# Performance work log

Measured on AMD Instinct MI355X. Metric: run time of the kernel, lower is better.

Reference implementation:

```python
import jax, jax.numpy as jnp
import numpy as np

N_NODES = 50000
N_EDGES = 600000
D = 128
L = 3


def setup_inputs() -> dict:
    key = jax.random.key(0)
    ks = jax.random.split(key, 6)
    x = jax.random.normal(ks[0], (N_NODES, D), dtype=jnp.float32)
    edge_index = jax.random.randint(ks[1], (2, N_EDGES), 0, N_NODES, dtype=jnp.int64)
    # Glorot-ish scale for 128x128 linears
    s = 1.0 / np.sqrt(D)
    W_l = jax.random.normal(ks[2], (L, D, D), dtype=jnp.float32) * s
    b_l = jnp.zeros((L, D), dtype=jnp.float32)
    W_r = jax.random.normal(ks[3], (L, D, D), dtype=jnp.float32) * s
    W_out = jax.random.normal(ks[4], (D, 1), dtype=jnp.float32) * s
    b_out = jnp.zeros((1,), dtype=jnp.float32)
    return {"x": x, "edge_index": edge_index, "W_l": W_l, "b_l": b_l,
            "W_r": W_r, "W_out": W_out, "b_out": b_out}


def reference(x, edge_index, W_l, b_l, W_r, W_out, b_out):
    # PyG SAGEConv (aggr='mean', root_weight=True):
    #   out_i = lin_l(mean_{j: (j->i)} x_j) + lin_r(x_i)
    src = edge_index[0]
    dst = edge_index[1]
    n = x.shape[0]
    deg = jax.ops.segment_sum(jnp.ones(src.shape, x.dtype), dst, num_segments=n)
    inv_deg = (1.0 / jnp.maximum(deg, 1.0))[:, None]  # [N,1]
    h = x
    for i in range(W_l.shape[0]):  # fixed small layer count
        agg = jax.ops.segment_sum(h[src], dst, num_segments=n) * inv_deg  # [N,D]
        h = agg @ W_l[i] + b_l[i] + h @ W_r[i]
        h = jax.nn.relu(h)  # dropout is identity at eval (p=0.0)
    return (h @ W_out + b_out)[:, 0]  # squeeze(-1) -> [N]
```

## Files before the change

### kernel.cpp

```cpp
#include <hip/hip_runtime.h>

#define N_NODES 50000
#define N_EDGES 600000
#define D 128
#define NLAYERS 3
#define ELL_W 64

typedef __attribute__((ext_vector_type(8))) short short8;
typedef __attribute__((ext_vector_type(4))) float floatx4;

__device__ __forceinline__ float bf_lo(unsigned u) { return __uint_as_float(u << 16); }
__device__ __forceinline__ float bf_hi(unsigned u) { return __uint_as_float(u & 0xffff0000u); }
__device__ __forceinline__ unsigned short f2bf(float f) {
    unsigned u = __float_as_uint(f);
    return (unsigned short)((u + 0x7fffu + ((u >> 16) & 1u)) >> 16);
}


#define CVT_A (N_NODES * D / 4)
#define CVT_B (NLAYERS * D * 256)
#define CVT_D (N_NODES * ELL_W / 4)
#define CVT_TOTAL (CVT_A + CVT_B + N_NODES + CVT_D)

__global__ void cvt_init_kernel(const float* __restrict__ x, const float* __restrict__ Wl,
                                const float* __restrict__ Wr,
                                unsigned short* __restrict__ xb,
                                unsigned short* __restrict__ hb1,
                                unsigned short* __restrict__ hb2,
                                unsigned short* __restrict__ WtF,
                                int* __restrict__ cursor, int* __restrict__ ell) {
    int i = blockIdx.x * blockDim.x + threadIdx.x;
    if (i < CVT_A) {
        float4 v = ((const float4*)x)[i];
        ushort4 o;
        o.x = f2bf(v.x); o.y = f2bf(v.y); o.z = f2bf(v.z); o.w = f2bf(v.w);
        ((ushort4*)xb)[i] = o;
    } else if (i < CVT_A + CVT_B) {
        int t = i - CVT_A;
        int l = t >> 15;
        int r = t & 32767;
        int f = r >> 3;
        int ii = r & 7;
        int jkt = f >> 6;
        int lane = f & 63;
        int j = jkt >> 3;
        int kt = jkt & 7;
        int half = lane & 15;
        int quad = lane >> 4;
        int n = j * 16 + half;
        int k = kt * 32 + quad * 8 + ii;
        float v = (k < D) ? Wl[(size_t)l * D * D + (size_t)k * D + n]
                          : Wr[(size_t)l * D * D + (size_t)(k - D) * D + n];
        WtF[t] = f2bf(v);
    } else if (i < CVT_A + CVT_B + N_NODES) {
        int j = i - (CVT_A + CVT_B);
        cursor[j] = 0;
        if (j < D) {
            xb[(size_t)N_NODES * D + j] = 0;
            hb1[(size_t)N_NODES * D + j] = 0;
            hb2[(size_t)N_NODES * D + j] = 0;
        }
    } else if (i < CVT_TOTAL) {
        int t = i - (CVT_A + CVT_B + N_NODES);
        int4 s = {N_NODES, N_NODES, N_NODES, N_NODES};
        ((int4*)ell)[t] = s;
    }
}


__global__ void fill_kernel(const int* __restrict__ src, const int* __restrict__ dst,
                            int* __restrict__ cursor, int* __restrict__ ell) {
    int e = blockIdx.x * blockDim.x + threadIdx.x;
    if (e < N_EDGES) {
        int d_ = dst[e];
        int pos = atomicAdd(&cursor[d_], 1);
        if (pos < ELL_W) ell[(size_t)d_ * ELL_W + pos] = src[e];
    }
}


template <bool LAST>
__global__ __launch_bounds__(256) void fused_layer_kernel(
    const unsigned short* __restrict__ hin,
    const int* __restrict__ degc, const int* __restrict__ ell,
    const unsigned short* __restrict__ WtF, const float* __restrict__ bias,
    unsigned short* __restrict__ hout,
    const float* __restrict__ Wout, const float* __restrict__ bout,
    float* __restrict__ out) {
    __shared__ union {
        unsigned short a[32 * 256];
        unsigned short c[32][136];
        float red[32][4];
    } sh;

    int m0 = blockIdx.x * 32;
    int tid = threadIdx.x;

    #pragma unroll
    for (int it = 0; it < 2; ++it) {
        int t = it * 256 + tid;
        int rl = t >> 4;
        int c = t & 15;
        int row = min(m0 + rl, N_NODES - 1);
        uint4 v = *((const uint4*)(hin + (size_t)row * D + c * 8));
        int chunk = (16 + c) ^ (rl & 7);
        *((uint4*)&sh.a[rl * 256 + chunk * 8]) = v;
    }

    {
        int grp = tid >> 4;
        int q = tid & 15;
        for (int half_ = 0; half_ < 2; ++half_) {
            int nl = grp + half_ * 16;
            int node = m0 + nl;
            float a[8] = {0.f, 0.f, 0.f, 0.f, 0.f, 0.f, 0.f, 0.f};
            float b[8] = {0.f, 0.f, 0.f, 0.f, 0.f, 0.f, 0.f, 0.f};
            float w = 0.f;
            if (node < N_NODES) {
                int d = min(degc[node], ELL_W);
                int pd = (d + 3) & ~3;
                int beg = node * ELL_W;
                for (int e = beg; e < beg + pd; e += 16) {
                    int cnt = min(beg + pd - e, 16);
                    int idx = ell[e + q];
                    for (int j = 0; j < cnt; j += 4) {
                        int s0 = __shfl(idx, j + 0, 16);
                        int s1 = __shfl(idx, j + 1, 16);
                        int s2 = __shfl(idx, j + 2, 16);
                        int s3 = __shfl(idx, j + 3, 16);
                        uint4 v0 = *((const uint4*)(hin + (size_t)s0 * D + q * 8));
                        uint4 v1 = *((const uint4*)(hin + (size_t)s1 * D + q * 8));
                        uint4 v2 = *((const uint4*)(hin + (size_t)s2 * D + q * 8));
                        uint4 v3 = *((const uint4*)(hin + (size_t)s3 * D + q * 8));
                        a[0] += bf_lo(v0.x); a[1] += bf_hi(v0.x);
                        a[2] += bf_lo(v0.y); a[3] += bf_hi(v0.y);
                        a[4] += bf_lo(v0.z); a[5] += bf_hi(v0.z);
                        a[6] += bf_lo(v0.w); a[7] += bf_hi(v0.w);
                        b[0] += bf_lo(v1.x); b[1] += bf_hi(v1.x);
                        b[2] += bf_lo(v1.y); b[3] += bf_hi(v1.y);
                        b[4] += bf_lo(v1.z); b[5] += bf_hi(v1.z);
                        b[6] += bf_lo(v1.w); b[7] += bf_hi(v1.w);
                        a[0] += bf_lo(v2.x); a[1] += bf_hi(v2.x);
                        a[2] += bf_lo(v2.y); a[3] += bf_hi(v2.y);
                        a[4] += bf_lo(v2.z); a[5] += bf_hi(v2.z);
                        a[6] += bf_lo(v2.w); a[7] += bf_hi(v2.w);
                        b[0] += bf_lo(v3.x); b[1] += bf_hi(v3.x);
                        b[2] += bf_lo(v3.y); b[3] += bf_hi(v3.y);
                        b[4] += bf_lo(v3.z); b[5] += bf_hi(v3.z);
                        b[6] += bf_lo(v3.w); b[7] += bf_hi(v3.w);
                    }
                }
                w = 1.0f / (float)max(d, 1);
            }
            uint4 o;
            o.x = (unsigned)f2bf((a[0] + b[0]) * w) | ((unsigned)f2bf((a[1] + b[1]) * w) << 16);
            o.y = (unsigned)f2bf((a[2] + b[2]) * w) | ((unsigned)f2bf((a[3] + b[3]) * w) << 16);
            o.z = (unsigned)f2bf((a[4] + b[4]) * w) | ((unsigned)f2bf((a[5] + b[5]) * w) << 16);
            o.w = (unsigned)f2bf((a[6] + b[6]) * w) | ((unsigned)f2bf((a[7] + b[7]) * w) << 16);
            int chunk = q ^ (nl & 7);
            *((uint4*)&sh.a[nl * 256 + chunk * 8]) = o;
        }
    }
    __syncthreads();

    int wv = tid >> 6;
    int lane = tid & 63;
    int half = lane & 15;
    int quad = lane >> 4;

    floatx4 acc[2][2];
    #pragma unroll
    for (int mt = 0; mt < 2; mt++)
        #pragma unroll
        for (int jj = 0; jj < 2; jj++)
            acc[mt][jj] = (floatx4){0.f, 0.f, 0.f, 0.f};

    const short8* Bf = (const short8*)WtF;
    #pragma unroll
    for (int kt = 0; kt < 8; kt++) {
        int ch = (kt * 4 + quad) ^ (half & 7);
        short8 a0 = *((const short8*)&sh.a[half * 256 + ch * 8]);
        short8 a1 = *((const short8*)&sh.a[(16 + half) * 256 + ch * 8]);
        #pragma unroll
        for (int jj = 0; jj < 2; jj++) {
            int j = wv * 2 + jj;
            short8 b = Bf[(j * 8 + kt) * 64 + lane];
            acc[0][jj] = __builtin_amdgcn_mfma_f32_16x16x32_bf16(a0, b, acc[0][jj], 0, 0, 0);
            acc[1][jj] = __builtin_amdgcn_mfma_f32_16x16x32_bf16(a1, b, acc[1][jj], 0, 0, 0);
        }
    }
    __syncthreads();

    if (!LAST) {
        #pragma unroll
        for (int jj = 0; jj < 2; jj++) {
            int col = (wv * 2 + jj) * 16 + half;
            float bv = bias[col];
            #pragma unroll
            for (int mt = 0; mt < 2; mt++)
                #pragma unroll
                for (int r = 0; r < 4; r++)
                    sh.c[mt * 16 + quad * 4 + r][col] = f2bf(fmaxf(acc[mt][jj][r] + bv, 0.f));
        }
        __syncthreads();
        #pragma unroll
        for (int it = 0; it < 2; ++it) {
            int t = it * 256 + tid;
            int rl = t >> 4;
            int c = t & 15;
            int row = m0 + rl;
            if (row < N_NODES)
                *((uint4*)(hout + (size_t)row * D + c * 8)) = *((const uint4*)&sh.c[rl][c * 8]);
        }
    } else {
        float vout[2][4] = {{0.f, 0.f, 0.f, 0.f}, {0.f, 0.f, 0.f, 0.f}};
        #pragma unroll
        for (int jj = 0; jj < 2; jj++) {
            int col = (wv * 2 + jj) * 16 + half;
            float bv = bias[col];
            float wo = Wout[col];
            #pragma unroll
            for (int mt = 0; mt < 2; mt++)
                #pragma unroll
                for (int r = 0; r < 4; r++)
                    vout[mt][r] += fmaxf(acc[mt][jj][r] + bv, 0.f) * wo;
        }
        #pragma unroll
        for (int off = 1; off < 16; off <<= 1) {
            #pragma unroll
            for (int mt = 0; mt < 2; mt++)
                #pragma unroll
                for (int r = 0; r < 4; r++)
                    vout[mt][r] += __shfl_xor(vout[mt][r], off, 64);
        }
        if (half == 0) {
            #pragma unroll
            for (int mt = 0; mt < 2; mt++)
                #pragma unroll
                for (int r = 0; r < 4; r++)
                    sh.red[mt * 16 + quad * 4 + r][wv] = vout[mt][r];
        }
        __syncthreads();
        if (tid < 32) {
            int row = m0 + tid;
            if (row < N_NODES)
                out[row] = sh.red[tid][0] + sh.red[tid][1] +
                           sh.red[tid][2] + sh.red[tid][3] + bout[0];
        }
    }
}


extern "C" void kernel_launch(void* const* d_in, const int* in_sizes, int n_in,
                              void* d_out, int out_size, void* d_ws, size_t ws_size,
                              hipStream_t stream) {
    const float* x     = (const float*)d_in[0];
    const int*   edge  = (const int*)d_in[1];
    const float* W_l   = (const float*)d_in[2];
    const float* b_l   = (const float*)d_in[3];
    const float* W_r   = (const float*)d_in[4];
    const float* W_out = (const float*)d_in[5];
    const float* b_out = (const float*)d_in[6];
    float* out = (float*)d_out;

    char* ws = (char*)d_ws;
    size_t off = 0;
    auto alloc = [&](size_t bytes) -> void* {
        void* p = ws + off;
        off += (bytes + 255) & ~(size_t)255;
        return p;
    };
    unsigned short* xb  = (unsigned short*)alloc((size_t)(N_NODES + 1) * D * 2);
    unsigned short* hb1 = (unsigned short*)alloc((size_t)(N_NODES + 1) * D * 2);
    unsigned short* hb2 = (unsigned short*)alloc((size_t)(N_NODES + 1) * D * 2);
    unsigned short* WtF = (unsigned short*)alloc((size_t)NLAYERS * D * 256 * 2);
    int* cursor = (int*)alloc((size_t)N_NODES * sizeof(int));
    int* ell    = (int*)alloc((size_t)N_NODES * ELL_W * sizeof(int));

    const int* src = edge;
    const int* dst = edge + N_EDGES;

    cvt_init_kernel<<<(CVT_TOTAL + 255) / 256, 256, 0, stream>>>(
        x, W_l, W_r, xb, hb1, hb2, WtF, cursor, ell);
    fill_kernel<<<(N_EDGES + 255) / 256, 256, 0, stream>>>(src, dst, cursor, ell);

    const int grid = (N_NODES + 31) / 32;

    fused_layer_kernel<false><<<grid, 256, 0, stream>>>(
        xb, cursor, ell, WtF, b_l, hb1, W_out, b_out, out);
    fused_layer_kernel<false><<<grid, 256, 0, stream>>>(
        hb1, cursor, ell, WtF + (size_t)1 * D * 256, b_l + 1 * D, hb2, W_out, b_out, out);
    fused_layer_kernel<true><<<grid, 256, 0, stream>>>(
        hb2, cursor, ell, WtF + (size_t)2 * D * 256, b_l + 2 * D, hb1, W_out, b_out, out);
}
```

Measured before the change: 210.8 us.

## Fuse ELL fill into init kernel and mask padded neighbor slots

Merges the conversion/init kernel and the edge-fill kernel into one launch, moving cursor zeroing to a memset so the fill atomics can share the launch. It drops the full ELL sentinel initialization (N_NODES*64 ints written) and instead masks padded slots in the gather loop by substituting the zero row index. This saves a large memory write and one kernel launch, at the cost of a few extra selects per gather step. It relies on the memset finishing before the fused kernel, which stream ordering guarantees.

```diff
diff --git a/kernel.cpp b/kernel.cpp
--- a/kernel.cpp
+++ b/kernel.cpp
@@ -17,26 +17,27 @@
 }
 
 
-#define CVT_A (N_NODES * D / 4)
-#define CVT_B (NLAYERS * D * 256)
-#define CVT_D (N_NODES * ELL_W / 4)
-#define CVT_TOTAL (CVT_A + CVT_B + N_NODES + CVT_D)
-
-__global__ void cvt_init_kernel(const float* __restrict__ x, const float* __restrict__ Wl,
-                                const float* __restrict__ Wr,
-                                unsigned short* __restrict__ xb,
-                                unsigned short* __restrict__ hb1,
-                                unsigned short* __restrict__ hb2,
-                                unsigned short* __restrict__ WtF,
-                                int* __restrict__ cursor, int* __restrict__ ell) {
+#define SEC_A (N_NODES * D / 4)
+#define SEC_B (SEC_A + NLAYERS * D * 256)
+#define SEC_C (SEC_B + 256)
+#define SEC_TOT (SEC_C + N_EDGES)
+
+__global__ void init_fill_kernel(const float* __restrict__ x, const float* __restrict__ Wl,
+                                 const float* __restrict__ Wr,
+                                 const int* __restrict__ src, const int* __restrict__ dst,
+                                 unsigned short* __restrict__ xb,
+                                 unsigned short* __restrict__ hb1,
+                                 unsigned short* __restrict__ hb2,
+                                 unsigned short* __restrict__ WtF,
+                                 int* __restrict__ cursor, int* __restrict__ ell) {
     int i = blockIdx.x * blockDim.x + threadIdx.x;
-    if (i < CVT_A) {
+    if (i < SEC_A) {
         float4 v = ((const float4*)x)[i];
         ushort4 o;
         o.x = f2bf(v.x); o.y = f2bf(v.y); o.z = f2bf(v.z); o.w = f2bf(v.w);
         ((ushort4*)xb)[i] = o;
-    } else if (i < CVT_A + CVT_B) {
-        int t = i - CVT_A;
+    } else if (i < SEC_B) {
+        int t = i - SEC_A;
         int l = t >> 15;
         int r = t & 32767;
         int f = r >> 3;
@@ -52,26 +53,15 @@
         float v = (k < D) ? Wl[(size_t)l * D * D + (size_t)k * D + n]
                           : Wr[(size_t)l * D * D + (size_t)(k - D) * D + n];
         WtF[t] = f2bf(v);
-    } else if (i < CVT_A + CVT_B + N_NODES) {
-        int j = i - (CVT_A + CVT_B);
-        cursor[j] = 0;
+    } else if (i < SEC_C) {
+        int j = i - SEC_B;
         if (j < D) {
             xb[(size_t)N_NODES * D + j] = 0;
             hb1[(size_t)N_NODES * D + j] = 0;
             hb2[(size_t)N_NODES * D + j] = 0;
         }
-    } else if (i < CVT_TOTAL) {
-        int t = i - (CVT_A + CVT_B + N_NODES);
-        int4 s = {N_NODES, N_NODES, N_NODES, N_NODES};
-        ((int4*)ell)[t] = s;
-    }
-}
-
-
-__global__ void fill_kernel(const int* __restrict__ src, const int* __restrict__ dst,
-                            int* __restrict__ cursor, int* __restrict__ ell) {
-    int e = blockIdx.x * blockDim.x + threadIdx.x;
-    if (e < N_EDGES) {
+    } else if (i < SEC_TOT) {
+        int e = i - SEC_C;
         int d_ = dst[e];
         int pos = atomicAdd(&cursor[d_], 1);
         if (pos < ELL_W) ell[(size_t)d_ * ELL_W + pos] = src[e];
@@ -119,15 +109,19 @@
             if (node < N_NODES) {
                 int d = min(degc[node], ELL_W);
                 int pd = (d + 3) & ~3;
-                int beg = node * ELL_W;
-                for (int e = beg; e < beg + pd; e += 16) {
-                    int cnt = min(beg + pd - e, 16);
-                    int idx = ell[e + q];
+                int base = node * ELL_W;
+                for (int e = 0; e < pd; e += 16) {
+                    int cnt = min(pd - e, 16);
+                    int idx = ell[base + e + q];
                     for (int j = 0; j < cnt; j += 4) {
+                        int rem = d - e - j;
                         int s0 = __shfl(idx, j + 0, 16);
                         int s1 = __shfl(idx, j + 1, 16);
                         int s2 = __shfl(idx, j + 2, 16);
                         int s3 = __shfl(idx, j + 3, 16);
+                        s1 = (1 < rem) ? s1 : N_NODES;
+                        s2 = (2 < rem) ? s2 : N_NODES;
+                        s3 = (3 < rem) ? s3 : N_NODES;
                         uint4 v0 = *((const uint4*)(hin + (size_t)s0 * D + q * 8));
                         uint4 v1 = *((const uint4*)(hin + (size_t)s1 * D + q * 8));
                         uint4 v2 = *((const uint4*)(hin + (size_t)s2 * D + q * 8));
@@ -280,9 +274,9 @@
     const int* src = edge;
     const int* dst = edge + N_EDGES;
 
-    cvt_init_kernel<<<(CVT_TOTAL + 255) / 256, 256, 0, stream>>>(
-        x, W_l, W_r, xb, hb1, hb2, WtF, cursor, ell);
-    fill_kernel<<<(N_EDGES + 255) / 256, 256, 0, stream>>>(src, dst, cursor, ell);
+    hipMemsetAsync(cursor, 0, (size_t)N_NODES * sizeof(int), stream);
+    init_fill_kernel<<<(SEC_TOT + 255) / 256, 256, 0, stream>>>(
+        x, W_l, W_r, src, dst, xb, hb1, hb2, WtF, cursor, ell);
 
     const int grid = (N_NODES + 31) / 32;
 
```

New measurement: 220.0 us. +4.4%, slower.
